# Kernel tuning notes

Hardware: AMD Instinct MI355X
Metric: run time of the kernel (lower is better)

The kernel has to match this reference:

```python
import jax, jax.numpy as jnp
import numpy as np

B, N, M = 2, 4096, 4096
QUERY_DIM = 1024
CONTEXT_DIM = 1024
HEADS = 16
DIM_HEAD = 64
INNER = HEADS * DIM_HEAD


def setup_inputs() -> dict:
    key = jax.random.key(0)
    ks = jax.random.split(key, 7)
    s = 0.02
    return {
        "x": jax.random.normal(ks[0], (B, N, QUERY_DIM), dtype=jnp.float32),
        "context": jax.random.normal(ks[1], (B, M, CONTEXT_DIM), dtype=jnp.float32),
        "Wq": jax.random.normal(ks[2], (QUERY_DIM, INNER), dtype=jnp.float32) * s,
        "Wk": jax.random.normal(ks[3], (CONTEXT_DIM, INNER), dtype=jnp.float32) * s,
        "Wv": jax.random.normal(ks[4], (CONTEXT_DIM, INNER), dtype=jnp.float32) * s,
        "Wo": jax.random.normal(ks[5], (INNER, QUERY_DIM), dtype=jnp.float32) * s,
        "bo": jnp.zeros((QUERY_DIM,), dtype=jnp.float32),
    }


def reference(x, context, Wq, Wk, Wv, Wo, bo):
    scale = DIM_HEAD ** -0.5
    # projections, then split heads: b n (h d) -> b h n d
    q = (x @ Wq).reshape(B, N, HEADS, DIM_HEAD).transpose(0, 2, 1, 3)
    k = (context @ Wk).reshape(B, M, HEADS, DIM_HEAD).transpose(0, 2, 1, 3)
    v = (context @ Wv).reshape(B, M, HEADS, DIM_HEAD).transpose(0, 2, 1, 3)
    attn = jnp.einsum('bhnd,bhmd->bhnm', q, k) * scale  # [B,H,N,M]
    attn = jax.nn.softmax(attn, axis=-1)
    out = jnp.einsum('bhnm,bhmd->bhnd', attn, v)
    out = out.transpose(0, 2, 1, 3).reshape(B, N, INNER)  # b h n d -> b n (h d)
    return out @ Wo + bo  # dropout(p=0) is identity
```

## Files before the change

### kernel.cpp

```cpp
#include <hip/hip_runtime.h>

using f16    = _Float16;
using f16x2  = __attribute__((ext_vector_type(2))) _Float16;
using f16x4  = __attribute__((ext_vector_type(4))) _Float16;
using f16x8  = __attribute__((ext_vector_type(8))) _Float16;
using h16x2  = __attribute__((ext_vector_type(2))) __fp16;
using f32x4  = __attribute__((ext_vector_type(4))) float;
using f32x16 = __attribute__((ext_vector_type(16))) float;
using u32    = unsigned int;
using u32x4  = __attribute__((ext_vector_type(4))) u32;

#define DI __device__ __forceinline__

DI f16x4 pack4(float a, float b, float c, float d) {
  f16x2 lo = __builtin_bit_cast(f16x2, __builtin_amdgcn_cvt_pkrtz(a, b));
  f16x2 hi = __builtin_bit_cast(f16x2, __builtin_amdgcn_cvt_pkrtz(c, d));
  f16x4 r; r[0] = lo[0]; r[1] = lo[1]; r[2] = hi[0]; r[3] = hi[1];
  return r;
}

DI u32 pk32(float a, float b) {
  return __builtin_bit_cast(u32, __builtin_amdgcn_cvt_pkrtz(a, b));
}

DI float dot1(u32 wrd, float acc) {
#if __has_builtin(__builtin_amdgcn_fdot2)
  h16x2 one; one[0] = (__fp16)1.f; one[1] = (__fp16)1.f;
  return __builtin_amdgcn_fdot2(__builtin_bit_cast(h16x2, wrd), one, acc, false);
#else
  f16x2 p = __builtin_bit_cast(f16x2, wrd);
  return acc + (float)p[0] + (float)p[1];
#endif
}

DI void gll16(const void* g, void* l) {
  __builtin_amdgcn_global_load_lds((const __attribute__((address_space(1))) u32*)g,
                                   (__attribute__((address_space(3))) u32*)l, 16, 0, 0);
}

DI f16x8 ldfrag(const void* base, int row, int u4) {
  int phys = u4 ^ (row & 7);
  return *(const f16x8*)((const char*)base + row * 128 + phys * 16);
}

DI f32x4 mfma16(f16x8 a, f16x8 b, f32x4 c) {
  return __builtin_amdgcn_mfma_f32_16x16x32_f16(a, b, c, 0, 0, 0);
}
DI f32x16 mfma32(f16x8 a, f16x8 b, f32x16 c) {
  return __builtin_amdgcn_mfma_f32_32x32x16_f16(a, b, c, 0, 0, 0);
}

DI void softhalf(const f32x16& s, f16x8* bp2, float& lr) {
  f32x16 e;
#pragma unroll
  for (int i = 0; i < 16; ++i) e[i] = __builtin_amdgcn_exp2f(s[i]);
  u32 a[8];
#pragma unroll
  for (int i = 0; i < 8; ++i) a[i] = pk32(e[2 * i], e[2 * i + 1]);
  float s0 = lr;
#pragma unroll
  for (int i = 0; i < 8; ++i) s0 = dot1(a[i], s0);
  lr = s0;
  auto s02 = __builtin_amdgcn_permlane32_swap(a[0], a[2], false, false);
  auto s13 = __builtin_amdgcn_permlane32_swap(a[1], a[3], false, false);
  auto s46 = __builtin_amdgcn_permlane32_swap(a[4], a[6], false, false);
  auto s57 = __builtin_amdgcn_permlane32_swap(a[5], a[7], false, false);
  u32x4 w0 = {s02[0], s13[0], s02[1], s13[1]};
  u32x4 w1 = {s46[0], s57[0], s46[1], s57[1]};
  bp2[0] = __builtin_bit_cast(f16x8, w0);
  bp2[1] = __builtin_bit_cast(f16x8, w1);
}

__global__ void k_cvt2(const float* __restrict__ x, const float* __restrict__ ctx,
                       f16* __restrict__ dst, int n4) {
  int z = blockIdx.y;
  const float* s = z ? ctx : x;
  f16* d = dst + (size_t)z * 8192 * 1024;
  int i = blockIdx.x * blockDim.x + threadIdx.x;
  if (i < n4) {
    float4 v = ((const float4*)s)[i];
    ((f16x4*)d)[i] = pack4(v.x, v.y, v.z, v.w);
  }
}

__global__ void k_wt4(const float* __restrict__ Wq, const float* __restrict__ Wk,
                      const float* __restrict__ Wv, const float* __restrict__ Wo,
                      f16* __restrict__ WTb) {
  int z = blockIdx.z;
  const float* W = z == 0 ? Wq : z == 1 ? Wk : z == 2 ? Wv : Wo;
  f16* WT = WTb + (size_t)z * 1024 * 1024;
  __shared__ float tile[64][65];
  int k0 = blockIdx.y * 64, n0 = blockIdx.x * 64;
  int t = threadIdx.x;
#pragma unroll
  for (int p = 0; p < 4; ++p) {
    int r = p * 16 + (t >> 4);
    int c = (t & 15) * 4;
    float4 v = *(const float4*)&W[(size_t)(k0 + r) * 1024 + n0 + c];
    tile[r][c] = v.x; tile[r][c + 1] = v.y; tile[r][c + 2] = v.z; tile[r][c + 3] = v.w;
  }
  __syncthreads();
#pragma unroll
  for (int p = 0; p < 4; ++p) {
    int n = p * 16 + (t >> 4);
    int k = (t & 15) * 4;
    *(f16x4*)&WT[(size_t)(n0 + n) * 1024 + k0 + k] =
        pack4(tile[k][n], tile[k + 1][n], tile[k + 2][n], tile[k + 3][n]);
  }
}

template <int EPI>
__global__ __launch_bounds__(256) void k_gemm(const f16* __restrict__ A, const f16* __restrict__ Bt,
                                              void* __restrict__ Cp, const float* __restrict__ bias) {
  __shared__ __align__(16) char smem[65536];
  f16* sA = (f16*)smem;
  f16* sB = (f16*)(smem + 32768);
  const int tid = threadIdx.x, w = tid >> 6, lane = tid & 63;
  const int g = lane >> 4, l15 = lane & 15, l7 = lane & 7, l8 = lane >> 3;
  const int m0 = blockIdx.x * 128, n0 = blockIdx.y * 128;
  const int wm = w >> 1, wn = w & 1;
  const int uswz = l7 ^ l8;

  auto stage = [&](int kt, int bufi) {
    int kb = kt * 128;
#pragma unroll
    for (int q = 0; q < 4; ++q) {
      int row = w * 32 + q * 8 + l8;
      gll16((const char*)A + (size_t)(m0 + row) * 2048 + kb + uswz * 16,
            (char*)sA + bufi * 16384 + (w * 32 + q * 8) * 128);
      gll16((const char*)Bt + (size_t)(n0 + row) * 2048 + kb + uswz * 16,
            (char*)sB + bufi * 16384 + (w * 32 + q * 8) * 128);
    }
  };

  f32x4 acc[4][4] = {};
  stage(0, 0);
  for (int kt = 0; kt < 16; ++kt) {
    asm volatile("s_waitcnt vmcnt(0)" ::: "memory");
    __syncthreads();
    if (kt + 1 < 16) stage(kt + 1, (kt + 1) & 1);
    const f16* aL = (const f16*)((const char*)sA + (kt & 1) * 16384);
    const f16* bL = (const f16*)((const char*)sB + (kt & 1) * 16384);
#pragma unroll
    for (int kc = 0; kc < 2; ++kc) {
      f16x8 af[4], bf[4];
#pragma unroll
      for (int mi = 0; mi < 4; ++mi) af[mi] = ldfrag(aL, wm * 64 + mi * 16 + l15, kc * 4 + g);
#pragma unroll
      for (int ni = 0; ni < 4; ++ni) bf[ni] = ldfrag(bL, wn * 64 + ni * 16 + l15, kc * 4 + g);
#pragma unroll
      for (int mi = 0; mi < 4; ++mi)
#pragma unroll
        for (int ni = 0; ni < 4; ++ni) acc[mi][ni] = mfma16(af[mi], bf[ni], acc[mi][ni]);
    }
  }

  if (EPI == 2) {
    float* C = (float*)Cp;
    float bv[4];
#pragma unroll
    for (int ni = 0; ni < 4; ++ni) bv[ni] = bias[n0 + wn * 64 + ni * 16 + l15];
#pragma unroll
    for (int mi = 0; mi < 4; ++mi)
#pragma unroll
      for (int ni = 0; ni < 4; ++ni) {
        int col = n0 + wn * 64 + ni * 16 + l15;
#pragma unroll
        for (int i = 0; i < 4; ++i) {
          int row = m0 + wm * 64 + mi * 16 + g * 4 + i;
          C[(size_t)row * 1024 + col] = acc[mi][ni][i] + bv[ni];
        }
      }
    return;
  }

  __syncthreads();
  f16* Ct = (f16*)smem;
  if (EPI == 0 || EPI == 3) {
#pragma unroll
    for (int mi = 0; mi < 4; ++mi)
#pragma unroll
      for (int ni = 0; ni < 4; ++ni) {
        int col = wn * 64 + ni * 16 + l15;
#pragma unroll
        for (int i = 0; i < 4; ++i) Ct[(wm * 64 + mi * 16 + g * 4 + i) * 136 + col] = (f16)acc[mi][ni][i];
      }
    __syncthreads();
    if (EPI == 0) {
      f16* C = (f16*)Cp;
#pragma unroll
      for (int p = 0; p < 8; ++p) {
        int r = p * 16 + (tid >> 4), cu = tid & 15;
        f16x8 v = *(const f16x8*)((const char*)Ct + r * 272 + cu * 16);
        *(f16x8*)((char*)C + (size_t)(m0 + r) * 2048 + n0 * 2 + cu * 16) = v;
      }
    } else {
      int b = m0 >> 12, mmr = m0 & 4095;
#pragma unroll
      for (int p = 0; p < 8; ++p) {
        int r = p * 16 + (tid >> 4), cu = tid & 15;
        f16x8 v = *(const f16x8*)((const char*)Ct + r * 272 + cu * 16);
        int kvr = mmr + r;
        int h = (n0 >> 6) + (cu >> 3);
        size_t off = ((size_t)((b * 16 + h) * 64 + (kvr >> 6))) * 8192 + (cu & 7) * 1024 + (kvr & 63) * 16;
        *(f16x8*)((char*)Cp + off) = v;
      }
    }
  } else {
#pragma unroll
    for (int mi = 0; mi < 4; ++mi)
#pragma unroll
      for (int ni = 0; ni < 4; ++ni) {
        int n = wn * 64 + ni * 16 + l15;
        int mcol = wm * 64 + mi * 16 + g * 4;
        *(f16x4*)&Ct[n * 136 + mcol] =
            pack4(acc[mi][ni][0], acc[mi][ni][1], acc[mi][ni][2], acc[mi][ni][3]);
      }
    __syncthreads();
    int b = m0 >> 12, mm = m0 & 4095;
#pragma unroll
    for (int p = 0; p < 8; ++p) {
      int r = p * 16 + (tid >> 4), cu = tid & 15;
      f16x8 v = *(const f16x8*)((const char*)Ct + r * 272 + cu * 16);
      int h = (n0 + r) >> 6, d = (n0 + r) & 63;
      size_t off = ((size_t)((b * 16 + h) * 64 + (mm >> 6) + (cu >> 3))) * 8192 + (cu & 7) * 1024 + d * 16;
      *(f16x8*)((char*)Cp + off) = v;
    }
  }
}

__global__ __launch_bounds__(256, 2) void k_attn(const f16* __restrict__ Qh, const f16* __restrict__ Ks,
                                                 const f16* __restrict__ Vs, f16* __restrict__ Oh) {
  __shared__ __align__(16) char smem[32768];
  const int tid = threadIdx.x, w = tid >> 6, lane = tid & 63;
  const int hi = lane >> 5, c = lane & 31, l7 = lane & 7, l8 = lane >> 3;
  const int bid = blockIdx.x;
  const int bh = (bid & 7) * 4 + (bid >> 7);
  const int qc = (bid >> 3) & 15;
  const int b = bh >> 4, h = bh & 15;
  const int rowB = b * 4096;
  const int qrow0 = rowB + qc * 256 + w * 64;
  const size_t tb = (size_t)bh * 64 * 8192;

  const int offA0 = hi * 1024 + c * 16;
  const int offA1 = offA0 + 512;

  const f16 ce = (f16)0.18033688f;
  f16x8 bQ0[4], bQ1[4];
#pragma unroll
  for (int ks = 0; ks < 4; ++ks) {
    f16x8 r0 = *(const f16x8*)(Qh + (size_t)(qrow0 + c) * 1024 + h * 64 + ks * 16 + hi * 8);
    f16x8 r1 = *(const f16x8*)(Qh + (size_t)(qrow0 + 32 + c) * 1024 + h * 64 + ks * 16 + hi * 8);
#pragma unroll
    for (int e = 0; e < 8; ++e) { r0[e] *= ce; r1[e] *= ce; }
    bQ0[ks] = r0; bQ1[ks] = r1;
  }

  const f32x16 Z = {};
  f32x16 acc00 = {}, acc01 = {}, acc10 = {}, acc11 = {};
  float lrow0 = 0.f, lrow1 = 0.f;

  f16x8 kf[8], vf[8];
  auto loadK = [&](int t) {
    const char* pK = (const char*)Ks + tb + (size_t)t * 8192;
#pragma unroll
    for (int ks = 0; ks < 4; ++ks) {
      kf[ks * 2]     = *(const f16x8*)(pK + ks * 2048 + offA0);
      kf[ks * 2 + 1] = *(const f16x8*)(pK + ks * 2048 + offA1);
    }
  };
  auto loadV = [&](int t) {
    const char* pV = (const char*)Vs + tb + (size_t)t * 8192;
#pragma unroll
    for (int ks = 0; ks < 4; ++ks) {
      vf[ks * 2]     = *(const f16x8*)(pV + ks * 2048 + offA0);
      vf[ks * 2 + 1] = *(const f16x8*)(pV + ks * 2048 + offA1);
    }
  };

  loadK(0);
  loadV(0);
#pragma unroll 1
  for (int t = 0; t < 64; ++t) {
    int tn = (t + 1) & 63;

    __builtin_amdgcn_s_setprio(1);
    f32x16 st00 = mfma32(kf[0], bQ0[0], Z);
    f32x16 st01 = mfma32(kf[0], bQ1[0], Z);
#pragma unroll
    for (int ks = 1; ks < 4; ++ks) {
      st00 = mfma32(kf[ks * 2], bQ0[ks], st00);
      st01 = mfma32(kf[ks * 2], bQ1[ks], st01);
    }
    f32x16 st10 = mfma32(kf[1], bQ0[0], Z);
    f32x16 st11 = mfma32(kf[1], bQ1[0], Z);
#pragma unroll
    for (int ks = 1; ks < 4; ++ks) {
      st10 = mfma32(kf[ks * 2 + 1], bQ0[ks], st10);
      st11 = mfma32(kf[ks * 2 + 1], bQ1[ks], st11);
    }
    __builtin_amdgcn_s_setprio(0);
    __builtin_amdgcn_sched_barrier(0);

    loadK(tn);
    __builtin_amdgcn_sched_barrier(0);

    f16x8 bpA[4], bpB[4];
    softhalf(st00, &bpA[0], lrow0);
    softhalf(st01, &bpB[0], lrow1);
    __builtin_amdgcn_sched_barrier(0);

    __builtin_amdgcn_s_setprio(1);
    acc00 = mfma32(vf[0], bpA[0], acc00);
    acc01 = mfma32(vf[0], bpB[0], acc01);
    acc10 = mfma32(vf[1], bpA[0], acc10);
    acc11 = mfma32(vf[1], bpB[0], acc11);
    acc00 = mfma32(vf[2], bpA[1], acc00);
    acc01 = mfma32(vf[2], bpB[1], acc01);
    acc10 = mfma32(vf[3], bpA[1], acc10);
    acc11 = mfma32(vf[3], bpB[1], acc11);
    __builtin_amdgcn_s_setprio(0);
    __builtin_amdgcn_sched_barrier(0);

    softhalf(st10, &bpA[2], lrow0);
    softhalf(st11, &bpB[2], lrow1);
    __builtin_amdgcn_sched_barrier(0);

    __builtin_amdgcn_s_setprio(1);
    acc00 = mfma32(vf[4], bpA[2], acc00);
    acc01 = mfma32(vf[4], bpB[2], acc01);
    acc10 = mfma32(vf[5], bpA[2], acc10);
    acc11 = mfma32(vf[5], bpB[2], acc11);
    acc00 = mfma32(vf[6], bpA[3], acc00);
    acc01 = mfma32(vf[6], bpB[3], acc01);
    acc10 = mfma32(vf[7], bpA[3], acc10);
    acc11 = mfma32(vf[7], bpB[3], acc11);
    __builtin_amdgcn_s_setprio(0);
    __builtin_amdgcn_sched_barrier(0);

    loadV(tn);
    __builtin_amdgcn_sched_barrier(0);
  }

  float inv0, inv1;
  {
    auto r2 = __builtin_amdgcn_permlane32_swap(__builtin_bit_cast(u32, lrow0),
                                               __builtin_bit_cast(u32, lrow0), false, false);
    inv0 = 1.0f / (__builtin_bit_cast(float, r2[0]) + __builtin_bit_cast(float, r2[1]));
  }
  {
    auto r2 = __builtin_amdgcn_permlane32_swap(__builtin_bit_cast(u32, lrow1),
                                               __builtin_bit_cast(u32, lrow1), false, false);
    inv1 = 1.0f / (__builtin_bit_cast(float, r2[0]) + __builtin_bit_cast(float, r2[1]));
  }

  char* myO = (char*)smem + w * 8192;
#pragma unroll
  for (int rb = 0; rb < 2; ++rb) {
    float iv = rb ? inv1 : inv0;
    int r = rb * 32 + c;
#pragma unroll
    for (int dt = 0; dt < 2; ++dt) {
      const f32x16& A = rb ? (dt ? acc11 : acc01) : (dt ? acc10 : acc00);
#pragma unroll
      for (int q8 = 0; q8 < 4; ++q8) {
        f16x4 hv = pack4(A[q8 * 4] * iv, A[q8 * 4 + 1] * iv, A[q8 * 4 + 2] * iv, A[q8 * 4 + 3] * iv);
        int slot = dt * 4 + q8;
        *(f16x4*)(myO + r * 128 + ((slot ^ (r & 7)) * 16) + hi * 8) = hv;
      }
    }
  }
#pragma unroll
  for (int p = 0; p < 8; ++p) {
    int r = p * 8 + l8;
    f16x8 v = *(const f16x8*)(myO + r * 128 + ((l7 ^ (r & 7)) * 16));
    *(f16x8*)((char*)Oh + ((size_t)(qrow0 + r) * 1024 + h * 64) * 2 + l7 * 16) = v;
  }
}

extern "C" void kernel_launch(void* const* d_in, const int* in_sizes, int n_in,
                              void* d_out, int out_size, void* d_ws, size_t ws_size,
                              hipStream_t stream) {
  const float* x   = (const float*)d_in[0];
  const float* ctx = (const float*)d_in[1];
  const float* Wq  = (const float*)d_in[2];
  const float* Wk  = (const float*)d_in[3];
  const float* Wv  = (const float*)d_in[4];
  const float* Wo  = (const float*)d_in[5];
  const float* bo  = (const float*)d_in[6];
  float* out = (float*)d_out;

  const size_t NR = 8192, KD = 1024;
  if (ws_size < (size_t)(5 * NR * KD * 2 + 4 * KD * KD * 2)) return;

  char* ws = (char*)d_ws;
  f16* xh  = (f16*)ws;
  f16* ch  = xh + NR * KD;
  f16* WqT = ch + NR * KD;
  f16* WkT = WqT + KD * KD;
  f16* WvT = WkT + KD * KD;
  f16* WoT = WvT + KD * KD;
  f16* Qh  = WoT + KD * KD;
  f16* Ks  = Qh + NR * KD;
  f16* Vs  = Ks + NR * KD;
  f16* Oh  = xh;

  int n4 = (int)(NR * KD / 4);
  k_cvt2<<<dim3((n4 + 255) / 256, 2), dim3(256), 0, stream>>>(x, ctx, xh, n4);
  k_wt4<<<dim3(16, 16, 4), dim3(256), 0, stream>>>(Wq, Wk, Wv, Wo, WqT);

  dim3 gg(64, 8), gb(256);
  k_gemm<0><<<gg, gb, 0, stream>>>(xh, WqT, (void*)Qh, nullptr);
  k_gemm<3><<<gg, gb, 0, stream>>>(ch, WkT, (void*)Ks, nullptr);
  k_gemm<1><<<gg, gb, 0, stream>>>(ch, WvT, (void*)Vs, nullptr);

  k_attn<<<dim3(512), dim3(256), 0, stream>>>(Qh, Ks, Vs, Oh);

  k_gemm<2><<<gg, gb, 0, stream>>>(Oh, WoT, (void*)out, bo);
}
```

Before: 281.7 us.

## Halve per-wave query rows in attention, double grid and occupancy, drop prefetch

Each attention wave now handles 32 query rows instead of 64, so the grid doubles to 1024 blocks and launch bounds allow 4 blocks per CU with half the shared memory. The software prefetch of the next K/V tile and the explicit sched barriers are removed; K and V are now loaded inside the iteration just before use. The goal is to lower register pressure and hide memory latency through more resident waves rather than manual pipelining. The cost is that each K/V tile is reused by half as many query rows, which doubles K/V global/L2 traffic, and in-wave latency hiding is lost.

```diff
diff --git a/kernel.cpp b/kernel.cpp
--- a/kernel.cpp
+++ b/kernel.cpp
@@ -229,152 +229,102 @@
   }
 }
 
-__global__ __launch_bounds__(256, 2) void k_attn(const f16* __restrict__ Qh, const f16* __restrict__ Ks,
+__global__ __launch_bounds__(256, 4) void k_attn(const f16* __restrict__ Qh, const f16* __restrict__ Ks,
                                                  const f16* __restrict__ Vs, f16* __restrict__ Oh) {
-  __shared__ __align__(16) char smem[32768];
+  __shared__ __align__(16) char smem[16384];
   const int tid = threadIdx.x, w = tid >> 6, lane = tid & 63;
   const int hi = lane >> 5, c = lane & 31, l7 = lane & 7, l8 = lane >> 3;
   const int bid = blockIdx.x;
-  const int bh = (bid & 7) * 4 + (bid >> 7);
-  const int qc = (bid >> 3) & 15;
+  const int bh = (bid & 7) * 4 + (bid >> 8);
+  const int qc = (bid >> 3) & 31;
   const int b = bh >> 4, h = bh & 15;
   const int rowB = b * 4096;
-  const int qrow0 = rowB + qc * 256 + w * 64;
+  const int qrow0 = rowB + qc * 128 + w * 32;
   const size_t tb = (size_t)bh * 64 * 8192;
 
   const int offA0 = hi * 1024 + c * 16;
   const int offA1 = offA0 + 512;
 
   const f16 ce = (f16)0.18033688f;
-  f16x8 bQ0[4], bQ1[4];
+  f16x8 bQ[4];
 #pragma unroll
   for (int ks = 0; ks < 4; ++ks) {
     f16x8 r0 = *(const f16x8*)(Qh + (size_t)(qrow0 + c) * 1024 + h * 64 + ks * 16 + hi * 8);
-    f16x8 r1 = *(const f16x8*)(Qh + (size_t)(qrow0 + 32 + c) * 1024 + h * 64 + ks * 16 + hi * 8);
-#pragma unroll
-    for (int e = 0; e < 8; ++e) { r0[e] *= ce; r1[e] *= ce; }
-    bQ0[ks] = r0; bQ1[ks] = r1;
+#pragma unroll
+    for (int e = 0; e < 8; ++e) r0[e] *= ce;
+    bQ[ks] = r0;
   }
 
   const f32x16 Z = {};
-  f32x16 acc00 = {}, acc01 = {}, acc10 = {}, acc11 = {};
-  float lrow0 = 0.f, lrow1 = 0.f;
-
-  f16x8 kf[8], vf[8];
-  auto loadK = [&](int t) {
+  f32x16 acc0 = {}, acc1 = {};
+  float lrow = 0.f;
+
+#pragma unroll 1
+  for (int t = 0; t < 64; ++t) {
     const char* pK = (const char*)Ks + tb + (size_t)t * 8192;
+    const char* pV = (const char*)Vs + tb + (size_t)t * 8192;
+
+    f16x8 kf[8];
 #pragma unroll
     for (int ks = 0; ks < 4; ++ks) {
       kf[ks * 2]     = *(const f16x8*)(pK + ks * 2048 + offA0);
       kf[ks * 2 + 1] = *(const f16x8*)(pK + ks * 2048 + offA1);
     }
-  };
-  auto loadV = [&](int t) {
-    const char* pV = (const char*)Vs + tb + (size_t)t * 8192;
+
+    __builtin_amdgcn_s_setprio(1);
+    f32x16 st0 = mfma32(kf[0], bQ[0], Z);
+    f32x16 st1 = mfma32(kf[1], bQ[0], Z);
+#pragma unroll
+    for (int ks = 1; ks < 4; ++ks) {
+      st0 = mfma32(kf[ks * 2], bQ[ks], st0);
+      st1 = mfma32(kf[ks * 2 + 1], bQ[ks], st1);
+    }
+    __builtin_amdgcn_s_setprio(0);
+
+    f16x8 vf[8];
 #pragma unroll
     for (int ks = 0; ks < 4; ++ks) {
       vf[ks * 2]     = *(const f16x8*)(pV + ks * 2048 + offA0);
       vf[ks * 2 + 1] = *(const f16x8*)(pV + ks * 2048 + offA1);
     }
-  };
-
-  loadK(0);
-  loadV(0);
-#pragma unroll 1
-  for (int t = 0; t < 64; ++t) {
-    int tn = (t + 1) & 63;
+
+    f16x8 bp[4];
+    softhalf(st0, &bp[0], lrow);
+    softhalf(st1, &bp[2], lrow);
 
     __builtin_amdgcn_s_setprio(1);
-    f32x16 st00 = mfma32(kf[0], bQ0[0], Z);
-    f32x16 st01 = mfma32(kf[0], bQ1[0], Z);
-#pragma unroll
-    for (int ks = 1; ks < 4; ++ks) {
-      st00 = mfma32(kf[ks * 2], bQ0[ks], st00);
-      st01 = mfma32(kf[ks * 2], bQ1[ks], st01);
-    }
-    f32x16 st10 = mfma32(kf[1], bQ0[0], Z);
-    f32x16 st11 = mfma32(kf[1], bQ1[0], Z);
-#pragma unroll
-    for (int ks = 1; ks < 4; ++ks) {
-      st10 = mfma32(kf[ks * 2 + 1], bQ0[ks], st10);
-      st11 = mfma32(kf[ks * 2 + 1], bQ1[ks], st11);
+#pragma unroll
+    for (int ks = 0; ks < 4; ++ks) {
+      acc0 = mfma32(vf[ks * 2], bp[ks], acc0);
+      acc1 = mfma32(vf[ks * 2 + 1], bp[ks], acc1);
     }
     __builtin_amdgcn_s_setprio(0);
-    __builtin_amdgcn_sched_barrier(0);
-
-    loadK(tn);
-    __builtin_amdgcn_sched_barrier(0);
-
-    f16x8 bpA[4], bpB[4];
-    softhalf(st00, &bpA[0], lrow0);
-    softhalf(st01, &bpB[0], lrow1);
-    __builtin_amdgcn_sched_barrier(0);
-
-    __builtin_amdgcn_s_setprio(1);
-    acc00 = mfma32(vf[0], bpA[0], acc00);
-    acc01 = mfma32(vf[0], bpB[0], acc01);
-    acc10 = mfma32(vf[1], bpA[0], acc10);
-    acc11 = mfma32(vf[1], bpB[0], acc11);
-    acc00 = mfma32(vf[2], bpA[1], acc00);
-    acc01 = mfma32(vf[2], bpB[1], acc01);
-    acc10 = mfma32(vf[3], bpA[1], acc10);
-    acc11 = mfma32(vf[3], bpB[1], acc11);
-    __builtin_amdgcn_s_setprio(0);
-    __builtin_amdgcn_sched_barrier(0);
-
-    softhalf(st10, &bpA[2], lrow0);
-    softhalf(st11, &bpB[2], lrow1);
-    __builtin_amdgcn_sched_barrier(0);
-
-    __builtin_amdgcn_s_setprio(1);
-    acc00 = mfma32(vf[4], bpA[2], acc00);
-    acc01 = mfma32(vf[4], bpB[2], acc01);
-    acc10 = mfma32(vf[5], bpA[2], acc10);
-    acc11 = mfma32(vf[5], bpB[2], acc11);
-    acc00 = mfma32(vf[6], bpA[3], acc00);
-    acc01 = mfma32(vf[6], bpB[3], acc01);
-    acc10 = mfma32(vf[7], bpA[3], acc10);
-    acc11 = mfma32(vf[7], bpB[3], acc11);
-    __builtin_amdgcn_s_setprio(0);
-    __builtin_amdgcn_sched_barrier(0);
-
-    loadV(tn);
-    __builtin_amdgcn_sched_barrier(0);
-  }
-
-  float inv0, inv1;
+  }
+
+  float inv;
   {
-    auto r2 = __builtin_amdgcn_permlane32_swap(__builtin_bit_cast(u32, lrow0),
-                                               __builtin_bit_cast(u32, lrow0), false, false);
-    inv0 = 1.0f / (__builtin_bit_cast(float, r2[0]) + __builtin_bit_cast(float, r2[1]));
-  }
-  {
-    auto r2 = __builtin_amdgcn_permlane32_swap(__builtin_bit_cast(u32, lrow1),
-                                               __builtin_bit_cast(u32, lrow1), false, false);
-    inv1 = 1.0f / (__builtin_bit_cast(float, r2[0]) + __builtin_bit_cast(float, r2[1]));
-  }
-
-  char* myO = (char*)smem + w * 8192;
-#pragma unroll
-  for (int rb = 0; rb < 2; ++rb) {
-    float iv = rb ? inv1 : inv0;
-    int r = rb * 32 + c;
-#pragma unroll
-    for (int dt = 0; dt < 2; ++dt) {
-      const f32x16& A = rb ? (dt ? acc11 : acc01) : (dt ? acc10 : acc00);
-#pragma unroll
-      for (int q8 = 0; q8 < 4; ++q8) {
-        f16x4 hv = pack4(A[q8 * 4] * iv, A[q8 * 4 + 1] * iv, A[q8 * 4 + 2] * iv, A[q8 * 4 + 3] * iv);
-        int slot = dt * 4 + q8;
-        *(f16x4*)(myO + r * 128 + ((slot ^ (r & 7)) * 16) + hi * 8) = hv;
-      }
-    }
-  }
-#pragma unroll
-  for (int p = 0; p < 8; ++p) {
-    int r = p * 8 + l8;
-    f16x8 v = *(const f16x8*)(myO + r * 128 + ((l7 ^ (r & 7)) * 16));
-    *(f16x8*)((char*)Oh + ((size_t)(qrow0 + r) * 1024 + h * 64) * 2 + l7 * 16) = v;
+    auto r2 = __builtin_amdgcn_permlane32_swap(__builtin_bit_cast(u32, lrow),
+                                               __builtin_bit_cast(u32, lrow), false, false);
+    inv = 1.0f / (__builtin_bit_cast(float, r2[0]) + __builtin_bit_cast(float, r2[1]));
+  }
+
+  char* myO = (char*)smem + w * 4096;
+  int r = c;
+#pragma unroll
+  for (int dt = 0; dt < 2; ++dt) {
+    const f32x16& A = dt ? acc1 : acc0;
+#pragma unroll
+    for (int q8 = 0; q8 < 4; ++q8) {
+      f16x4 hv = pack4(A[q8 * 4] * inv, A[q8 * 4 + 1] * inv, A[q8 * 4 + 2] * inv, A[q8 * 4 + 3] * inv);
+      int slot = dt * 4 + q8;
+      *(f16x4*)(myO + r * 128 + ((slot ^ (r & 7)) * 16) + hi * 8) = hv;
+    }
+  }
+#pragma unroll
+  for (int p = 0; p < 4; ++p) {
+    int rr = p * 8 + l8;
+    f16x8 v = *(const f16x8*)(myO + rr * 128 + ((l7 ^ (rr & 7)) * 16));
+    *(f16x8*)((char*)Oh + ((size_t)(qrow0 + rr) * 1024 + h * 64) * 2 + l7 * 16) = v;
   }
 }
 
@@ -414,7 +364,7 @@
   k_gemm<3><<<gg, gb, 0, stream>>>(ch, WkT, (void*)Ks, nullptr);
   k_gemm<1><<<gg, gb, 0, stream>>>(ch, WvT, (void*)Vs, nullptr);
 
-  k_attn<<<dim3(512), dim3(256), 0, stream>>>(Qh, Ks, Vs, Oh);
+  k_attn<<<dim3(1024), dim3(256), 0, stream>>>(Qh, Ks, Vs, Oh);
 
   k_gemm<2><<<gg, gb, 0, stream>>>(Oh, WoT, (void*)out, bo);
 }
```

New measurement: 360.2 us. 27.9% more time.
